# Kernel optimization log

Hardware: AMD Instinct MI355X
Metric: run time of the kernel (lower is better)

Reference implementation:

```python
import jax, jax.numpy as jnp
import numpy as np

NUM_EXPERTS = 8
VOCAB_SIZE = 100000
H = 1024
IE = 512  # intermediate_size // num_experts
B, S = 4, 8192


def setup_inputs() -> dict:
    key = jax.random.key(0)
    ks = jax.random.split(key, 8)
    return {
        "hidden_states": jax.random.normal(ks[0], (B, S, H), dtype=jnp.float32),
        "token_ids": jax.random.randint(ks[1], (B, S), 0, VOCAB_SIZE, dtype=jnp.int64),
        "gate_w": jax.random.normal(ks[2], (NUM_EXPERTS, H, IE), dtype=jnp.float32) * 0.02,
        "up_w": jax.random.normal(ks[3], (NUM_EXPERTS, H, IE), dtype=jnp.float32) * 0.02,
        "down_w": jax.random.normal(ks[4], (NUM_EXPERTS, IE, H), dtype=jnp.float32) * 0.02,
        "shared_gate_w": jax.random.normal(ks[5], (IE, H), dtype=jnp.float32) * 0.02,
        "shared_up_w": jax.random.normal(ks[6], (IE, H), dtype=jnp.float32) * 0.02,
        "shared_down_w": jax.random.normal(ks[7], (H, IE), dtype=jnp.float32) * 0.02,
    }


def reference(hidden_states, token_ids, gate_w, up_w, down_w,
              shared_gate_w, shared_up_w, shared_down_w):
    Bq, Sq, Hq = hidden_states.shape
    flat_x = hidden_states.reshape(-1, Hq)                    # [N, H]
    ids = jnp.clip(token_ids, 0, VOCAB_SIZE - 1).reshape(-1)  # [N]
    # token_to_expert buffer is arange(V) % E (no token_frequencies given)
    expert_ids = ids % NUM_EXPERTS                            # [N]

    # shared dense SwiGLU expert (torch Linear: x @ W.T)
    shared_out = (jax.nn.silu(flat_x @ shared_gate_w.T)
                  * (flat_x @ shared_up_w.T)) @ shared_down_w.T

    # routed experts: loop over the small fixed expert set, mask-combine
    routed_out = jnp.zeros_like(flat_x)
    for e in range(NUM_EXPERTS):
        mask = (expert_ids == e)[:, None]                     # [N, 1]
        inter = jax.nn.silu(flat_x @ gate_w[e]) * (flat_x @ up_w[e])  # [N, IE]
        routed_out = routed_out + jnp.where(mask, inter @ down_w[e], 0.0)

    return (routed_out + shared_out).reshape(Bq, Sq, Hq)
```

## Files before the change

### kernel.cpp

```cpp
#include <hip/hip_runtime.h>
#include <hip/hip_bf16.h>


#define N_TOK 32768
#define HD 1024
#define NE 8

typedef __attribute__((ext_vector_type(8))) short bf16x8;
typedef __attribute__((ext_vector_type(8))) unsigned short u16x8;
typedef __attribute__((ext_vector_type(4))) float f32x4;

__device__ __forceinline__ unsigned short f2bf(float f) {
  unsigned int x = __float_as_uint(f);
  x += 0x7fffu + ((x >> 16) & 1u);
  return (unsigned short)(x >> 16);
}

__device__ __forceinline__ void gld16(const unsigned short* g, unsigned short* l) {
  __builtin_amdgcn_global_load_lds(
      (const __attribute__((address_space(1))) unsigned int*)g,
      (__attribute__((address_space(3))) unsigned int*)l,
      16, 0, 0);
}

__device__ __forceinline__ int expert_of(int id) {
  int v = id < 0 ? 0 : (id > 99999 ? 99999 : id);
  return v & 7;
}

__global__ void k_zero(int* ctrl) {
  if (threadIdx.x < 16) ctrl[threadIdx.x] = 0;
}

__global__ void k_count(const int* __restrict__ ids, int* __restrict__ cnt) {
  __shared__ int l[NE];
  if (threadIdx.x < NE) l[threadIdx.x] = 0;
  __syncthreads();
  int t = blockIdx.x * 256 + threadIdx.x;
  atomicAdd(&l[expert_of(ids[t])], 1);
  __syncthreads();
  if (threadIdx.x < NE) atomicAdd(&cnt[threadIdx.x], l[threadIdx.x]);
}

__global__ void k_scan(const int* __restrict__ cnt, int* __restrict__ off) {
  if (threadIdx.x == 0 && blockIdx.x == 0) {
    int a = 0;
    for (int e = 0; e < NE; e++) { off[e] = a; a += (cnt[e] + 127) & ~127; }
    off[NE] = a;
  }
}

__global__ void k_fill(const int* __restrict__ ids, int* __restrict__ cursor,
                       const int* __restrict__ off, int* __restrict__ perm) {
  __shared__ int lcnt[NE], lbase[NE];
  if (threadIdx.x < NE) lcnt[threadIdx.x] = 0;
  __syncthreads();
  int t = blockIdx.x * 256 + threadIdx.x;
  int e = expert_of(ids[t]);
  int r = atomicAdd(&lcnt[e], 1);
  __syncthreads();
  if (threadIdx.x < NE)
    lbase[threadIdx.x] = atomicAdd(&cursor[threadIdx.x], lcnt[threadIdx.x]);
  __syncthreads();
  perm[off[e] + lbase[e] + r] = t;
}

__global__ void k_cvt_x(const float* __restrict__ src, unsigned short* __restrict__ dst) {
  size_t i = ((size_t)blockIdx.x * 256 + threadIdx.x) * 8;
  float4 a = *reinterpret_cast<const float4*>(src + i);
  float4 b = *reinterpret_cast<const float4*>(src + i + 4);
  u16x8 o;
  o[0]=f2bf(a.x); o[1]=f2bf(a.y); o[2]=f2bf(a.z); o[3]=f2bf(a.w);
  o[4]=f2bf(b.x); o[5]=f2bf(b.y); o[6]=f2bf(b.z); o[7]=f2bf(b.w);
  *reinterpret_cast<u16x8*>(dst + i) = o;
}

__device__ __forceinline__ int rowmap(int c, int mode) {
  if (mode == 0) return c;
  return ((c >> 4) << 5) + (c & 15) + (mode == 2 ? 16 : 0);
}

__global__ void k_transpose_cvt(const float* __restrict__ src0, unsigned short* __restrict__ dst0,
                                int C, int mode, size_t src_estride, size_t dst_estride) {
  const float* src = src0 + blockIdx.z * src_estride;
  unsigned short* dst = dst0 + blockIdx.z * dst_estride;
  __shared__ __attribute__((aligned(16))) float tile[32][33];
  int t = threadIdx.x;
  int r0 = blockIdx.y * 32, c0 = blockIdx.x * 32;
  int row = t >> 3, c4 = (t & 7) * 4;
  float4 v = *reinterpret_cast<const float4*>(src + (size_t)(r0 + row) * C + c0 + c4);
  tile[row][c4+0] = v.x; tile[row][c4+1] = v.y; tile[row][c4+2] = v.z; tile[row][c4+3] = v.w;
  __syncthreads();
  ushort4 o;
  o.x = f2bf(tile[c4+0][row]); o.y = f2bf(tile[c4+1][row]);
  o.z = f2bf(tile[c4+2][row]); o.w = f2bf(tile[c4+3][row]);
  int orow = rowmap(c0 + row, mode);
  *reinterpret_cast<ushort4*>(dst + (size_t)orow * HD + r0 + c4) = o;
}

__global__ void k_copy_cvt(const float* __restrict__ src, unsigned short* __restrict__ dst,
                           int cols, int mode, int dcol, size_t dst_estride) {
  size_t i = ((size_t)blockIdx.x * 256 + threadIdx.x) * 4;
  int r = (int)(i / cols), c = (int)(i % cols);
  int row = (mode == 0) ? r : (1024 + rowmap(r, mode));
  float4 v = *reinterpret_cast<const float4*>(src + i);
  ushort4 o; o.x=f2bf(v.x); o.y=f2bf(v.y); o.z=f2bf(v.z); o.w=f2bf(v.w);
  *reinterpret_cast<ushort4*>(dst + blockIdx.z * dst_estride
                              + (size_t)row * HD + dcol + c) = o;
}

__global__ __launch_bounds__(256, 3) void k_gu(
    const unsigned short* __restrict__ xbf,
    const unsigned short* __restrict__ W1,
    const int* __restrict__ perm, const int* __restrict__ cnt, const int* __restrict__ off,
    unsigned short* __restrict__ inter) {
  const int e = blockIdx.z;
  const int ce = cnt[e];
  const int m0 = blockIdx.y * 128;
  if (m0 >= ce) return;
  const int n0 = blockIdx.x * 128;
  const int oe = off[e];
  __shared__ __attribute__((aligned(16))) unsigned short smA[2 * 128 * 32];
  __shared__ __attribute__((aligned(16))) unsigned short smB[2 * 128 * 32];
  const int tid = threadIdx.x;
  const int lane = tid & 63;
  const int wv = tid >> 6;
  const int wm = wv >> 1, wn = wv & 1;

  const int srow = tid >> 2;
  const int skol = (tid & 3) * 8;
  const unsigned short* sa[2];
  const unsigned short* sb[2];
#pragma unroll
  for (int s = 0; s < 2; s++) {
    int i = m0 + s * 64 + srow;
    if (i > ce - 1) i = ce - 1;
    int tok = perm[oe + i];
    sa[s] = xbf + (size_t)tok * HD + skol;
    sb[s] = W1 + ((size_t)e << 21) + (size_t)(n0 + s * 64 + srow) * HD + skol;
  }

  f32x4 acc[4][4];
#pragma unroll
  for (int mi = 0; mi < 4; mi++)
#pragma unroll
    for (int ni = 0; ni < 4; ni++) acc[mi][ni] = (f32x4){0.f, 0.f, 0.f, 0.f};

  auto STAGE = [&](int b, int kt) {
    const int ko = kt * 32;
#pragma unroll
    for (int s = 0; s < 2; s++) {
      gld16(sa[s] + ko, smA + b * 4096 + s * 2048 + wv * 512);
      gld16(sb[s] + ko, smB + b * 4096 + s * 2048 + wv * 512);
    }
  };
  auto COMPUTE = [&](int b) {
    const unsigned short* A = smA + b * 4096;
    const unsigned short* B = smB + b * 4096;
    bf16x8 a[4], bb[4];
#pragma unroll
    for (int mi = 0; mi < 4; mi++)
      a[mi] = *reinterpret_cast<const bf16x8*>(A + (wm * 64 + mi * 16 + (lane & 15)) * 32 + (lane >> 4) * 8);
#pragma unroll
    for (int ni = 0; ni < 4; ni++)
      bb[ni] = *reinterpret_cast<const bf16x8*>(B + (wn * 64 + ni * 16 + (lane & 15)) * 32 + (lane >> 4) * 8);
#pragma unroll
    for (int mi = 0; mi < 4; mi++)
#pragma unroll
      for (int ni = 0; ni < 4; ni++)
        acc[mi][ni] = __builtin_amdgcn_mfma_f32_16x16x32_bf16(a[mi], bb[ni], acc[mi][ni], 0, 0, 0);
  };

  STAGE(0, 0);
  __syncthreads();
  int cur = 0;
#pragma unroll 1
  for (int kt = 0; kt < 31; kt++) {
    STAGE(cur ^ 1, kt + 1);
    COMPUTE(cur);
    __syncthreads();
    cur ^= 1;
  }
  COMPUTE(cur);

  const int colbase = (n0 + wn * 64) >> 1;
#pragma unroll
  for (int mi = 0; mi < 4; mi++)
#pragma unroll
    for (int p = 0; p < 2; p++)
#pragma unroll
      for (int r = 0; r < 4; r++) {
        int m = wm * 64 + mi * 16 + (lane >> 4) * 4 + r;
        float g = acc[mi][2 * p][r];
        float u = acc[mi][2 * p + 1][r];
        float sv = g / (1.f + __expf(-g)) * u;
        inter[(size_t)(oe + m0 + m) * HD + colbase + p * 16 + (lane & 15)] = f2bf(sv);
      }
}

__global__ __launch_bounds__(256, 3) void k_down(
    const unsigned short* __restrict__ inter,
    const unsigned short* __restrict__ Dt,
    const int* __restrict__ perm, const int* __restrict__ cnt, const int* __restrict__ off,
    float* __restrict__ out) {
  const int e = blockIdx.z;
  const int ce = cnt[e];
  const int m0 = blockIdx.y * 128;
  if (m0 >= ce) return;
  const int n0 = blockIdx.x * 128;
  const int oe = off[e];
  __shared__ __attribute__((aligned(16))) unsigned short smA[2 * 128 * 32];
  __shared__ __attribute__((aligned(16))) unsigned short smB[2 * 128 * 32];
  const int tid = threadIdx.x;
  const int lane = tid & 63;
  const int wv = tid >> 6;
  const int wm = wv >> 1, wn = wv & 1;

  const int srow = tid >> 2;
  const int skol = (tid & 3) * 8;
  const unsigned short* sa[2];
  const unsigned short* sb[2];
#pragma unroll
  for (int s = 0; s < 2; s++) {
    sa[s] = inter + (size_t)(oe + m0 + s * 64 + srow) * HD + skol;
    sb[s] = Dt + ((size_t)e << 20) + (size_t)(n0 + s * 64 + srow) * HD + skol;
  }

  f32x4 acc[4][4];
#pragma unroll
  for (int mi = 0; mi < 4; mi++)
#pragma unroll
    for (int ni = 0; ni < 4; ni++) acc[mi][ni] = (f32x4){0.f, 0.f, 0.f, 0.f};

  auto STAGE = [&](int b, int kt) {
    const int ko = kt * 32;
#pragma unroll
    for (int s = 0; s < 2; s++) {
      gld16(sa[s] + ko, smA + b * 4096 + s * 2048 + wv * 512);
      gld16(sb[s] + ko, smB + b * 4096 + s * 2048 + wv * 512);
    }
  };
  auto COMPUTE = [&](int b) {
    const unsigned short* A = smA + b * 4096;
    const unsigned short* B = smB + b * 4096;
    bf16x8 a[4], bb[4];
#pragma unroll
    for (int mi = 0; mi < 4; mi++)
      a[mi] = *reinterpret_cast<const bf16x8*>(A + (wm * 64 + mi * 16 + (lane & 15)) * 32 + (lane >> 4) * 8);
#pragma unroll
    for (int ni = 0; ni < 4; ni++)
      bb[ni] = *reinterpret_cast<const bf16x8*>(B + (wn * 64 + ni * 16 + (lane & 15)) * 32 + (lane >> 4) * 8);
#pragma unroll
    for (int mi = 0; mi < 4; mi++)
#pragma unroll
      for (int ni = 0; ni < 4; ni++)
        acc[mi][ni] = __builtin_amdgcn_mfma_f32_16x16x32_bf16(a[mi], bb[ni], acc[mi][ni], 0, 0, 0);
  };

  STAGE(0, 0);
  __syncthreads();
  int cur = 0;
#pragma unroll 1
  for (int kt = 0; kt < 31; kt++) {
    STAGE(cur ^ 1, kt + 1);
    COMPUTE(cur);
    __syncthreads();
    cur ^= 1;
  }
  COMPUTE(cur);

#pragma unroll
  for (int mi = 0; mi < 4; mi++)
#pragma unroll
    for (int r = 0; r < 4; r++) {
      int m = wm * 64 + mi * 16 + (lane >> 4) * 4 + r;
      int gm = m0 + m;
      if (gm < ce) {
        int t = perm[oe + gm];
#pragma unroll
        for (int ni = 0; ni < 4; ni++)
          out[(size_t)t * HD + n0 + wn * 64 + ni * 16 + (lane & 15)] = acc[mi][ni][r];
      }
    }
}

__global__ __launch_bounds__(256) void k_naive(
    const float* __restrict__ x, const int* __restrict__ ids,
    const float* __restrict__ gw, const float* __restrict__ uw, const float* __restrict__ dw,
    const float* __restrict__ sgw, const float* __restrict__ suw, const float* __restrict__ sdw,
    float* __restrict__ out) {
  const int t = blockIdx.x;
  const int tid = threadIdx.x;
  __shared__ float sx[1024];
  __shared__ float si[1024];
  for (int i = tid; i < 1024; i += 256) sx[i] = x[(size_t)t * 1024 + i];
  const int e = expert_of(ids[t]);
  __syncthreads();
  const float* gwe = gw + (size_t)e * 1024 * 512;
  const float* uwe = uw + (size_t)e * 1024 * 512;
  for (int j = tid; j < 512; j += 256) {
    float g = 0, u = 0, sg = 0, su = 0;
    for (int k = 0; k < 1024; k++) {
      float xv = sx[k];
      g += xv * gwe[(size_t)k * 512 + j];
      u += xv * uwe[(size_t)k * 512 + j];
      sg += xv * sgw[(size_t)j * 1024 + k];
      su += xv * suw[(size_t)j * 1024 + k];
    }
    si[j] = g / (1.f + __expf(-g)) * u;
    si[512 + j] = sg / (1.f + __expf(-sg)) * su;
  }
  __syncthreads();
  const float* dwe = dw + (size_t)e * 512 * 1024;
  for (int n = tid; n < 1024; n += 256) {
    float a = 0;
    for (int k = 0; k < 512; k++)
      a += si[k] * dwe[(size_t)k * 1024 + n] + si[512 + k] * sdw[(size_t)n * 512 + k];
    out[(size_t)t * 1024 + n] = a;
  }
}

extern "C" void kernel_launch(void* const* d_in, const int* in_sizes, int n_in,
                              void* d_out, int out_size, void* d_ws, size_t ws_size,
                              hipStream_t stream) {
  const float* x = (const float*)d_in[0];
  const int* ids = (const int*)d_in[1];
  const float* gw = (const float*)d_in[2];
  const float* uw = (const float*)d_in[3];
  const float* dw = (const float*)d_in[4];
  const float* sgw = (const float*)d_in[5];
  const float* suw = (const float*)d_in[6];
  const float* sdw = (const float*)d_in[7];
  float* out = (float*)d_out;

  const size_t REQ = 186908672ull;
  if (ws_size < REQ) {
    k_naive<<<N_TOK, 256, 0, stream>>>(x, ids, gw, uw, dw, sgw, suw, sdw, out);
    return;
  }

  char* ws = (char*)d_ws;
  int* ctrl = (int*)ws;
  int* perm = (int*)(ws + 1024);
  unsigned short* xbf = (unsigned short*)(ws + 262144);
  unsigned short* W1 = (unsigned short*)(ws + 67371008ull);
  unsigned short* Dt = (unsigned short*)(ws + 100925440ull);
  unsigned short* inter = (unsigned short*)(ws + 117702656ull);

  k_zero<<<1, 64, 0, stream>>>(ctrl);
  k_count<<<128, 256, 0, stream>>>(ids, ctrl);
  k_scan<<<1, 64, 0, stream>>>(ctrl, ctrl + 16);
  k_fill<<<128, 256, 0, stream>>>(ids, ctrl + 8, ctrl + 16, perm);
  k_cvt_x<<<16384, 256, 0, stream>>>(x, xbf);
  k_transpose_cvt<<<dim3(16, 32, 8), 256, 0, stream>>>(gw, W1, 512, 1,
                                                       (size_t)1024 * 512, (size_t)1 << 21);
  k_transpose_cvt<<<dim3(16, 32, 8), 256, 0, stream>>>(uw, W1, 512, 2,
                                                       (size_t)1024 * 512, (size_t)1 << 21);
  k_transpose_cvt<<<dim3(32, 16, 8), 256, 0, stream>>>(dw, Dt, 1024, 0,
                                                       (size_t)512 * 1024, (size_t)1 << 20);
  k_copy_cvt<<<dim3(512, 1, 8), 256, 0, stream>>>(sgw, W1, 1024, 1, 0, (size_t)1 << 21);
  k_copy_cvt<<<dim3(512, 1, 8), 256, 0, stream>>>(suw, W1, 1024, 2, 0, (size_t)1 << 21);
  k_copy_cvt<<<dim3(512, 1, 8), 256, 0, stream>>>(sdw, Dt, 512, 0, 512, (size_t)1 << 20);
  k_gu<<<dim3(16, 256, 8), 256, 0, stream>>>(xbf, W1, perm, ctrl, ctrl + 16, inter);
  k_down<<<dim3(8, 256, 8), 256, 0, stream>>>(inter, Dt, perm, ctrl, ctrl + 16, out);
}
```

Baseline: 376.7 us.

## Triple-buffer LDS pipeline with manual waitcnt and fragment-ordered shared layout

Both grouped GEMM kernels (gate/up and down) move from a double-buffered LDS pipeline to a three-stage ring buffer. Two k-tiles are prefetched ahead, and synchronization uses explicit s_waitcnt vmcnt plus raw s_barrier instead of __syncthreads. The staging lane mapping is changed so LDS holds data in MFMA fragment order, making each fragment read a contiguous lane*8 access that should avoid bank conflicts. s_setprio is raised around the MFMA block. Shared memory grows to 48KB per block, which may reduce occupancy from the launch-bounds target of 3 blocks per CU.

```diff
diff --git a/kernel.cpp b/kernel.cpp
--- a/kernel.cpp
+++ b/kernel.cpp
@@ -9,6 +9,8 @@
 typedef __attribute__((ext_vector_type(8))) short bf16x8;
 typedef __attribute__((ext_vector_type(8))) unsigned short u16x8;
 typedef __attribute__((ext_vector_type(4))) float f32x4;
+
+#define BAR() asm volatile("s_barrier" ::: "memory")
 
 __device__ __forceinline__ unsigned short f2bf(float f) {
   unsigned int x = __float_as_uint(f);
@@ -120,25 +122,20 @@
   if (m0 >= ce) return;
   const int n0 = blockIdx.x * 128;
   const int oe = off[e];
-  __shared__ __attribute__((aligned(16))) unsigned short smA[2 * 128 * 32];
-  __shared__ __attribute__((aligned(16))) unsigned short smB[2 * 128 * 32];
+  __shared__ __attribute__((aligned(16))) unsigned short sm[24576];
   const int tid = threadIdx.x;
   const int lane = tid & 63;
   const int wv = tid >> 6;
   const int wm = wv >> 1, wn = wv & 1;
 
-  const int srow = tid >> 2;
-  const int skol = (tid & 3) * 8;
-  const unsigned short* sa[2];
-  const unsigned short* sb[2];
-#pragma unroll
-  for (int s = 0; s < 2; s++) {
-    int i = m0 + s * 64 + srow;
-    if (i > ce - 1) i = ce - 1;
-    int tok = perm[oe + i];
-    sa[s] = xbf + (size_t)tok * HD + skol;
-    sb[s] = W1 + ((size_t)e << 21) + (size_t)(n0 + s * 64 + srow) * HD + skol;
-  }
+  const int srw = wv * 16 + (lane & 15);
+  const int srk = ((lane >> 4) & 3) * 8;
+  int ia = m0 + srw;        if (ia > ce - 1) ia = ce - 1;
+  int ib = m0 + 64 + srw;   if (ib > ce - 1) ib = ce - 1;
+  const unsigned short* pA0 = xbf + (size_t)perm[oe + ia] * HD + srk;
+  const unsigned short* pA1 = xbf + (size_t)perm[oe + ib] * HD + srk;
+  const unsigned short* pB0 = W1 + ((size_t)e << 21) + (size_t)(n0 + srw) * HD + srk;
+  const unsigned short* pB1 = W1 + ((size_t)e << 21) + (size_t)(n0 + 64 + srw) * HD + srk;
 
   f32x4 acc[4][4];
 #pragma unroll
@@ -148,40 +145,46 @@
 
   auto STAGE = [&](int b, int kt) {
     const int ko = kt * 32;
-#pragma unroll
-    for (int s = 0; s < 2; s++) {
-      gld16(sa[s] + ko, smA + b * 4096 + s * 2048 + wv * 512);
-      gld16(sb[s] + ko, smB + b * 4096 + s * 2048 + wv * 512);
-    }
+    unsigned short* la = sm + b * 8192 + wv * 512;
+    unsigned short* lb = sm + b * 8192 + 4096 + wv * 512;
+    gld16(pA0 + ko, la);
+    gld16(pA1 + ko, la + 2048);
+    gld16(pB0 + ko, lb);
+    gld16(pB1 + ko, lb + 2048);
   };
   auto COMPUTE = [&](int b) {
-    const unsigned short* A = smA + b * 4096;
-    const unsigned short* B = smB + b * 4096;
+    const unsigned short* A = sm + b * 8192;
+    const unsigned short* B = A + 4096;
     bf16x8 a[4], bb[4];
 #pragma unroll
     for (int mi = 0; mi < 4; mi++)
-      a[mi] = *reinterpret_cast<const bf16x8*>(A + (wm * 64 + mi * 16 + (lane & 15)) * 32 + (lane >> 4) * 8);
+      a[mi] = *reinterpret_cast<const bf16x8*>(A + (wm * 4 + mi) * 512 + lane * 8);
 #pragma unroll
     for (int ni = 0; ni < 4; ni++)
-      bb[ni] = *reinterpret_cast<const bf16x8*>(B + (wn * 64 + ni * 16 + (lane & 15)) * 32 + (lane >> 4) * 8);
+      bb[ni] = *reinterpret_cast<const bf16x8*>(B + (wn * 4 + ni) * 512 + lane * 8);
+    __builtin_amdgcn_s_setprio(1);
 #pragma unroll
     for (int mi = 0; mi < 4; mi++)
 #pragma unroll
       for (int ni = 0; ni < 4; ni++)
         acc[mi][ni] = __builtin_amdgcn_mfma_f32_16x16x32_bf16(a[mi], bb[ni], acc[mi][ni], 0, 0, 0);
+    __builtin_amdgcn_s_setprio(0);
   };
 
-  STAGE(0, 0);
-  __syncthreads();
-  int cur = 0;
+  STAGE(0, 0); STAGE(1, 1);
+  int bn = 2, bc = 0;
 #pragma unroll 1
-  for (int kt = 0; kt < 31; kt++) {
-    STAGE(cur ^ 1, kt + 1);
-    COMPUTE(cur);
-    __syncthreads();
-    cur ^= 1;
-  }
-  COMPUTE(cur);
+  for (int kt = 0; kt < 30; kt++) {
+    STAGE(bn, kt + 2);
+    asm volatile("s_waitcnt vmcnt(8)" ::: "memory");
+    BAR();
+    COMPUTE(bc);
+    BAR();
+    bn = bn == 2 ? 0 : bn + 1;
+    bc = bc == 2 ? 0 : bc + 1;
+  }
+  asm volatile("s_waitcnt vmcnt(4)" ::: "memory"); BAR(); COMPUTE(0); BAR();
+  asm volatile("s_waitcnt vmcnt(0)" ::: "memory"); BAR(); COMPUTE(1);
 
   const int colbase = (n0 + wn * 64) >> 1;
 #pragma unroll
@@ -209,22 +212,18 @@
   if (m0 >= ce) return;
   const int n0 = blockIdx.x * 128;
   const int oe = off[e];
-  __shared__ __attribute__((aligned(16))) unsigned short smA[2 * 128 * 32];
-  __shared__ __attribute__((aligned(16))) unsigned short smB[2 * 128 * 32];
+  __shared__ __attribute__((aligned(16))) unsigned short sm[24576];
   const int tid = threadIdx.x;
   const int lane = tid & 63;
   const int wv = tid >> 6;
   const int wm = wv >> 1, wn = wv & 1;
 
-  const int srow = tid >> 2;
-  const int skol = (tid & 3) * 8;
-  const unsigned short* sa[2];
-  const unsigned short* sb[2];
-#pragma unroll
-  for (int s = 0; s < 2; s++) {
-    sa[s] = inter + (size_t)(oe + m0 + s * 64 + srow) * HD + skol;
-    sb[s] = Dt + ((size_t)e << 20) + (size_t)(n0 + s * 64 + srow) * HD + skol;
-  }
+  const int srw = wv * 16 + (lane & 15);
+  const int srk = ((lane >> 4) & 3) * 8;
+  const unsigned short* pA0 = inter + (size_t)(oe + m0 + srw) * HD + srk;
+  const unsigned short* pA1 = inter + (size_t)(oe + m0 + 64 + srw) * HD + srk;
+  const unsigned short* pB0 = Dt + ((size_t)e << 20) + (size_t)(n0 + srw) * HD + srk;
+  const unsigned short* pB1 = Dt + ((size_t)e << 20) + (size_t)(n0 + 64 + srw) * HD + srk;
 
   f32x4 acc[4][4];
 #pragma unroll
@@ -234,40 +233,46 @@
 
   auto STAGE = [&](int b, int kt) {
     const int ko = kt * 32;
-#pragma unroll
-    for (int s = 0; s < 2; s++) {
-      gld16(sa[s] + ko, smA + b * 4096 + s * 2048 + wv * 512);
-      gld16(sb[s] + ko, smB + b * 4096 + s * 2048 + wv * 512);
-    }
+    unsigned short* la = sm + b * 8192 + wv * 512;
+    unsigned short* lb = sm + b * 8192 + 4096 + wv * 512;
+    gld16(pA0 + ko, la);
+    gld16(pA1 + ko, la + 2048);
+    gld16(pB0 + ko, lb);
+    gld16(pB1 + ko, lb + 2048);
   };
   auto COMPUTE = [&](int b) {
-    const unsigned short* A = smA + b * 4096;
-    const unsigned short* B = smB + b * 4096;
+    const unsigned short* A = sm + b * 8192;
+    const unsigned short* B = A + 4096;
     bf16x8 a[4], bb[4];
 #pragma unroll
     for (int mi = 0; mi < 4; mi++)
-      a[mi] = *reinterpret_cast<const bf16x8*>(A + (wm * 64 + mi * 16 + (lane & 15)) * 32 + (lane >> 4) * 8);
+      a[mi] = *reinterpret_cast<const bf16x8*>(A + (wm * 4 + mi) * 512 + lane * 8);
 #pragma unroll
     for (int ni = 0; ni < 4; ni++)
-      bb[ni] = *reinterpret_cast<const bf16x8*>(B + (wn * 64 + ni * 16 + (lane & 15)) * 32 + (lane >> 4) * 8);
+      bb[ni] = *reinterpret_cast<const bf16x8*>(B + (wn * 4 + ni) * 512 + lane * 8);
+    __builtin_amdgcn_s_setprio(1);
 #pragma unroll
     for (int mi = 0; mi < 4; mi++)
 #pragma unroll
       for (int ni = 0; ni < 4; ni++)
         acc[mi][ni] = __builtin_amdgcn_mfma_f32_16x16x32_bf16(a[mi], bb[ni], acc[mi][ni], 0, 0, 0);
+    __builtin_amdgcn_s_setprio(0);
   };
 
-  STAGE(0, 0);
-  __syncthreads();
-  int cur = 0;
+  STAGE(0, 0); STAGE(1, 1);
+  int bn = 2, bc = 0;
 #pragma unroll 1
-  for (int kt = 0; kt < 31; kt++) {
-    STAGE(cur ^ 1, kt + 1);
-    COMPUTE(cur);
-    __syncthreads();
-    cur ^= 1;
-  }
-  COMPUTE(cur);
+  for (int kt = 0; kt < 30; kt++) {
+    STAGE(bn, kt + 2);
+    asm volatile("s_waitcnt vmcnt(8)" ::: "memory");
+    BAR();
+    COMPUTE(bc);
+    BAR();
+    bn = bn == 2 ? 0 : bn + 1;
+    bc = bc == 2 ? 0 : bc + 1;
+  }
+  asm volatile("s_waitcnt vmcnt(4)" ::: "memory"); BAR(); COMPUTE(0); BAR();
+  asm volatile("s_waitcnt vmcnt(0)" ::: "memory"); BAR(); COMPUTE(1);
 
 #pragma unroll
   for (int mi = 0; mi < 4; mi++)
```

New measurement: 484.7 us. 28.7% more time.

## Flatten expert grid to compact tile list and merge weight-prep kernels

Applied to the files above, without the earlier changes.

The GEMM grids change from a fixed 256×8 y/z layout, where most blocks exit early, to a compact 1D list of 128-row tiles. Each block finds its expert by binary-like search over prefix tile offsets computed in k_scan. Six weight conversion/transposition launches are merged into one kernel. This cuts empty-block launch overhead and launch count, at the cost of a fixed MAXYT bound that assumes the padded tile total never exceeds 264.

```diff
diff --git a/kernel.cpp b/kernel.cpp
--- a/kernel.cpp
+++ b/kernel.cpp
@@ -5,6 +5,7 @@
 #define N_TOK 32768
 #define HD 1024
 #define NE 8
+#define MAXYT 264
 
 typedef __attribute__((ext_vector_type(8))) short bf16x8;
 typedef __attribute__((ext_vector_type(8))) unsigned short u16x8;
@@ -47,6 +48,7 @@
     int a = 0;
     for (int e = 0; e < NE; e++) { off[e] = a; a += (cnt[e] + 127) & ~127; }
     off[NE] = a;
+    for (int e = 0; e <= NE; e++) off[9 + e] = off[e] >> 7;
   }
 }
 
@@ -80,33 +82,53 @@
   return ((c >> 4) << 5) + (c & 15) + (mode == 2 ? 16 : 0);
 }
 
-__global__ void k_transpose_cvt(const float* __restrict__ src0, unsigned short* __restrict__ dst0,
-                                int C, int mode, size_t src_estride, size_t dst_estride) {
-  const float* src = src0 + blockIdx.z * src_estride;
-  unsigned short* dst = dst0 + blockIdx.z * dst_estride;
+__global__ void k_prep_w(const float* __restrict__ gw, const float* __restrict__ uw,
+                         const float* __restrict__ dw, const float* __restrict__ sgw,
+                         const float* __restrict__ suw, const float* __restrict__ sdw,
+                         unsigned short* __restrict__ W1, unsigned short* __restrict__ Dt) {
+  const int sec = blockIdx.x >> 12;
+  const int idx = blockIdx.x & 4095;
+  const int t = threadIdx.x;
+  const int e = idx >> 9;
   __shared__ __attribute__((aligned(16))) float tile[32][33];
-  int t = threadIdx.x;
-  int r0 = blockIdx.y * 32, c0 = blockIdx.x * 32;
-  int row = t >> 3, c4 = (t & 7) * 4;
-  float4 v = *reinterpret_cast<const float4*>(src + (size_t)(r0 + row) * C + c0 + c4);
-  tile[row][c4+0] = v.x; tile[row][c4+1] = v.y; tile[row][c4+2] = v.z; tile[row][c4+3] = v.w;
-  __syncthreads();
-  ushort4 o;
-  o.x = f2bf(tile[c4+0][row]); o.y = f2bf(tile[c4+1][row]);
-  o.z = f2bf(tile[c4+2][row]); o.w = f2bf(tile[c4+3][row]);
-  int orow = rowmap(c0 + row, mode);
-  *reinterpret_cast<ushort4*>(dst + (size_t)orow * HD + r0 + c4) = o;
-}
-
-__global__ void k_copy_cvt(const float* __restrict__ src, unsigned short* __restrict__ dst,
-                           int cols, int mode, int dcol, size_t dst_estride) {
-  size_t i = ((size_t)blockIdx.x * 256 + threadIdx.x) * 4;
-  int r = (int)(i / cols), c = (int)(i % cols);
-  int row = (mode == 0) ? r : (1024 + rowmap(r, mode));
-  float4 v = *reinterpret_cast<const float4*>(src + i);
-  ushort4 o; o.x=f2bf(v.x); o.y=f2bf(v.y); o.z=f2bf(v.z); o.w=f2bf(v.w);
-  *reinterpret_cast<ushort4*>(dst + blockIdx.z * dst_estride
-                              + (size_t)row * HD + dcol + c) = o;
+  if (sec < 3) {
+    const float* src; unsigned short* dst; int C, mode, bx, by;
+    size_t se, de;
+    if (sec == 0)      { src = gw; dst = W1; C = 512;  mode = 1; se = (size_t)1024*512; de = (size_t)1<<21; bx = idx & 15; by = (idx >> 4) & 31; }
+    else if (sec == 1) { src = uw; dst = W1; C = 512;  mode = 2; se = (size_t)1024*512; de = (size_t)1<<21; bx = idx & 15; by = (idx >> 4) & 31; }
+    else               { src = dw; dst = Dt; C = 1024; mode = 0; se = (size_t)512*1024; de = (size_t)1<<20; bx = idx & 31; by = (idx >> 5) & 15; }
+    src += e * se; dst += e * de;
+    int r0 = by * 32, c0 = bx * 32;
+    int row = t >> 3, c4 = (t & 7) * 4;
+    float4 v = *reinterpret_cast<const float4*>(src + (size_t)(r0 + row) * C + c0 + c4);
+    tile[row][c4+0] = v.x; tile[row][c4+1] = v.y; tile[row][c4+2] = v.z; tile[row][c4+3] = v.w;
+    __syncthreads();
+    ushort4 o;
+    o.x = f2bf(tile[c4+0][row]); o.y = f2bf(tile[c4+1][row]);
+    o.z = f2bf(tile[c4+2][row]); o.w = f2bf(tile[c4+3][row]);
+    int orow = rowmap(c0 + row, mode);
+    *reinterpret_cast<ushort4*>(dst + (size_t)orow * HD + r0 + c4) = o;
+  } else {
+    const float* src; unsigned short* dst; int mode, dcol, cols;
+    size_t de;
+    if (sec == 3)      { src = sgw; dst = W1; mode = 1; dcol = 0;   cols = 1024; de = (size_t)1<<21; }
+    else if (sec == 4) { src = suw; dst = W1; mode = 2; dcol = 0;   cols = 1024; de = (size_t)1<<21; }
+    else               { src = sdw; dst = Dt; mode = 0; dcol = 512; cols = 512;  de = (size_t)1<<20; }
+    int bx = idx & 511;
+    size_t i = ((size_t)bx * 256 + t) * 4;
+    int r = (int)(i / cols), c = (int)(i % cols);
+    int row = (mode == 0) ? r : (1024 + rowmap(r, mode));
+    float4 v = *reinterpret_cast<const float4*>(src + i);
+    ushort4 o; o.x=f2bf(v.x); o.y=f2bf(v.y); o.z=f2bf(v.z); o.w=f2bf(v.w);
+    *reinterpret_cast<ushort4*>(dst + e * de + (size_t)row * HD + dcol + c) = o;
+  }
+}
+
+__device__ __forceinline__ int tile_expert(const int* yb, int yt) {
+  int e = 0;
+#pragma unroll
+  for (int i = 1; i < NE; i++) if (yt >= yb[i]) e = i;
+  return e;
 }
 
 __global__ __launch_bounds__(256, 3) void k_gu(
@@ -114,9 +136,10 @@
     const unsigned short* __restrict__ W1,
     const int* __restrict__ perm, const int* __restrict__ cnt, const int* __restrict__ off,
     unsigned short* __restrict__ inter) {
-  const int e = blockIdx.z;
+  const int yt = blockIdx.y;
+  const int e = tile_expert(off + 9, yt);
   const int ce = cnt[e];
-  const int m0 = blockIdx.y * 128;
+  const int m0 = (yt - (off + 9)[e]) * 128;
   if (m0 >= ce) return;
   const int n0 = blockIdx.x * 128;
   const int oe = off[e];
@@ -203,9 +226,10 @@
     const unsigned short* __restrict__ Dt,
     const int* __restrict__ perm, const int* __restrict__ cnt, const int* __restrict__ off,
     float* __restrict__ out) {
-  const int e = blockIdx.z;
+  const int yt = blockIdx.y;
+  const int e = tile_expert(off + 9, yt);
   const int ce = cnt[e];
-  const int m0 = blockIdx.y * 128;
+  const int m0 = (yt - (off + 9)[e]) * 128;
   if (m0 >= ce) return;
   const int n0 = blockIdx.x * 128;
   const int oe = off[e];
@@ -352,15 +376,7 @@
   k_scan<<<1, 64, 0, stream>>>(ctrl, ctrl + 16);
   k_fill<<<128, 256, 0, stream>>>(ids, ctrl + 8, ctrl + 16, perm);
   k_cvt_x<<<16384, 256, 0, stream>>>(x, xbf);
-  k_transpose_cvt<<<dim3(16, 32, 8), 256, 0, stream>>>(gw, W1, 512, 1,
-                                                       (size_t)1024 * 512, (size_t)1 << 21);
-  k_transpose_cvt<<<dim3(16, 32, 8), 256, 0, stream>>>(uw, W1, 512, 2,
-                                                       (size_t)1024 * 512, (size_t)1 << 21);
-  k_transpose_cvt<<<dim3(32, 16, 8), 256, 0, stream>>>(dw, Dt, 1024, 0,
-                                                       (size_t)512 * 1024, (size_t)1 << 20);
-  k_copy_cvt<<<dim3(512, 1, 8), 256, 0, stream>>>(sgw, W1, 1024, 1, 0, (size_t)1 << 21);
-  k_copy_cvt<<<dim3(512, 1, 8), 256, 0, stream>>>(suw, W1, 1024, 2, 0, (size_t)1 << 21);
-  k_copy_cvt<<<dim3(512, 1, 8), 256, 0, stream>>>(sdw, Dt, 512, 0, 512, (size_t)1 << 20);
-  k_gu<<<dim3(16, 256, 8), 256, 0, stream>>>(xbf, W1, perm, ctrl, ctrl + 16, inter);
-  k_down<<<dim3(8, 256, 8), 256, 0, stream>>>(inter, Dt, perm, ctrl, ctrl + 16, out);
-}
+  k_prep_w<<<6 * 4096, 256, 0, stream>>>(gw, uw, dw, sgw, suw, sdw, W1, Dt);
+  k_gu<<<dim3(16, MAXYT), 256, 0, stream>>>(xbf, W1, perm, ctrl, ctrl + 16, inter);
+  k_down<<<dim3(8, MAXYT), 256, 0, stream>>>(inter, Dt, perm, ctrl, ctrl + 16, out);
+}
```

Result: faster. 368.7 us (-2.1%).
